# Kernel tuning notes

Measured on AMD Instinct MI355X. Metric: run time of the kernel, lower is better.

## Reference

```python
import jax, jax.numpy as jnp
import numpy as np

VOCAB, EMB, HID = 50000, 128, 256
B, T = 64, 512


def setup_inputs() -> dict:
    key = jax.random.key(0)
    ks = jax.random.split(key, 10)
    node = jax.random.randint(ks[0], (B, T, 2), 0, VOCAB, dtype=jnp.int32)
    rel = jax.random.randint(ks[1], (B, T, 3), 0, VOCAB, dtype=jnp.int32)
    father = jax.random.randint(ks[2], (B, T), 0, T, dtype=jnp.int32)
    mask = jnp.ones((B, T), jnp.float32)
    # parameters (PyTorch LSTM layout: gates ordered i,f,g,o)
    embedding = jax.random.normal(ks[3], (VOCAB, EMB), jnp.float32) * 1e-4
    W_ih = jax.random.uniform(ks[4], (4 * HID, 2 * EMB), jnp.float32, -0.02, 0.02)
    W_hh = jax.random.uniform(ks[5], (4 * HID, HID), jnp.float32, -0.02, 0.02)
    b_ih = jnp.zeros((4 * HID,), jnp.float32).at[HID:2 * HID].set(1.0)  # forget bias = 1
    b_hh = jnp.zeros((4 * HID,), jnp.float32)
    W_h = jax.random.normal(ks[6], (HID, HID), jnp.float32) * 0.02
    return {"src_gtr_seq_node": node, "src_gtr_seq_rel": rel,
            "src_gtr_seq_father": father, "src_gtr_seq_node_mask": mask,
            "embedding": embedding, "W_ih": W_ih, "W_hh": W_hh,
            "b_ih": b_ih, "b_hh": b_hh, "W_h": W_h}


def reference(src_gtr_seq_node, src_gtr_seq_rel, src_gtr_seq_father,
              src_gtr_seq_node_mask, embedding, W_ih, W_hh, b_ih, b_hh, W_h):
    node, rel, father, mask = (src_gtr_seq_node, src_gtr_seq_rel,
                               src_gtr_seq_father, src_gtr_seq_node_mask)
    Bn, Tn = node.shape[:2]
    H = W_hh.shape[1]
    t_idx = jnp.arange(Tn, dtype=jnp.int32)
    # valid parent at step t must point into memory slots [0..t]; -1 -> zero root slot
    father = jnp.minimum(father, (t_idx - 1)[None, :])
    # 'avg' mode: mean of first-2 node token embeddings, mean of rel token embeddings
    node_e = embedding[node].mean(axis=2)            # [B,T,E]
    rel_e = embedding[rel].mean(axis=2)              # [B,T,E]
    x = jnp.concatenate([node_e, rel_e], axis=-1)    # [B,T,2E]
    gx = jnp.einsum('bte,ge->btg', x, W_ih) + b_ih   # [B,T,4H] input-side gates
    barange = jnp.arange(Bn)
    h_mem0 = jnp.zeros((Tn + 1, Bn, H), x.dtype)     # slot 0 = zero state (root)
    c_mem0 = jnp.zeros((Tn + 1, Bn, H), x.dtype)

    def step(carry, inp):
        h_mem, c_mem = carry
        t, gx_t, f_t = inp
        h_prev = h_mem[f_t + 1, barange]             # parent gather [B,H]
        c_prev = c_mem[f_t + 1, barange]
        gates = gx_t + h_prev @ W_hh.T + b_hh        # [B,4H]
        i, f, g, o = jnp.split(gates, 4, axis=-1)
        c = jax.nn.sigmoid(f) * c_prev + jax.nn.sigmoid(i) * jnp.tanh(g)
        h = jax.nn.sigmoid(o) * jnp.tanh(c)
        return (h_mem.at[t + 1].set(h), c_mem.at[t + 1].set(c)), h

    (h_mem, c_mem), outs = jax.lax.scan(
        step, (h_mem0, c_mem0),
        (t_idx, gx.transpose(1, 0, 2), father.T))
    m = mask[:, :, None]
    encoder_outputs = outs.transpose(1, 0, 2) * m    # [B,T,H]
    encoder_feature = encoder_outputs.reshape(-1, H) @ W_h.T  # [B*T,H]
    h_max = (h_mem[1:].transpose(1, 0, 2) * m).max(axis=1)[None]  # [1,B,H]
    c_max = (c_mem[1:].transpose(1, 0, 2) * m).max(axis=1)[None]
    return encoder_outputs, encoder_feature, h_max, c_max
```

## Files before the change

### kernel.cpp

```cpp
#include <hip/hip_runtime.h>
#include <hip/hip_bf16.h>
#include <math.h>

#define NB 64
#define NT 512
#define NH 256
#define NG 1024

typedef __bf16 bf16x8 __attribute__((ext_vector_type(8)));
typedef float  f32x4  __attribute__((ext_vector_type(4)));

static __device__ __forceinline__ unsigned short f2bf(float x){
  __hip_bfloat16 h = __float2bfloat16(x);
  return __builtin_bit_cast(unsigned short, h);
}
static __device__ __forceinline__ float bf2f(unsigned short u){
  return __bfloat162float(__builtin_bit_cast(__hip_bfloat16, u));
}

#if __has_builtin(__builtin_amdgcn_sdot4)
#define SDOT4(a,b,c) __builtin_amdgcn_sdot4((a),(b),(c),false)
#else
static __device__ __forceinline__ int SDOT4(int a, int b, int c){
  c += ((a<<24)>>24)*((b<<24)>>24);
  c += ((a<<16)>>24)*((b<<16)>>24);
  c += ((a<< 8)>>24)*((b<< 8)>>24);
  c += ( a     >>24)*( b     >>24);
  return c;
}
#endif

#define BAR_LGKM() asm volatile("s_waitcnt lgkmcnt(0)\n\ts_barrier" ::: "memory")
#define BAR_ALL()  asm volatile("s_waitcnt vmcnt(0) lgkmcnt(0)\n\ts_barrier" ::: "memory")

#define PIN(x) asm volatile("" : "+v"(x))

static __device__ __forceinline__ float tanh_acc(float x){
  float ax = fabsf(x);
  if (ax < 0.04f){
    float x2 = x*x;
    return x * (1.0f + x2*(-(1.0f/3.0f) + x2*(2.0f/15.0f)));
  }
  float e = __expf(-2.0f*ax);
  float r = (1.0f - e) / (1.0f + e);
  return copysignf(r, x);
}
static __device__ __forceinline__ float sigm(float x){
  return 1.0f / (1.0f + __expf(-x));
}

#define HSCALE 1270000.0f
#define WSCALE 6350.0f
#define DQ_CONST (1.0f/(HSCALE*WSCALE))

__global__ __launch_bounds__(256) void k_prep(
    const float* __restrict__ Wih, const float* __restrict__ Whh,
    const float* __restrict__ Wh,  const float* __restrict__ bih,
    const float* __restrict__ bhh,
    unsigned short* __restrict__ wih_bf, unsigned short* __restrict__ wh_bf,
    int* __restrict__ wq, float* __restrict__ bias)
{
  int i = blockIdx.x*256 + threadIdx.x;
  wih_bf[i] = f2bf(Wih[i]);
  if (i < 65536){
    wh_bf[i] = f2bf(Wh[i]);
    float4 wv = *(const float4*)(Whh + (long)i*4);
    int q0 = (int)rintf(wv.x * WSCALE); q0 = max(-127, min(127, q0));
    int q1 = (int)rintf(wv.y * WSCALE); q1 = max(-127, min(127, q1));
    int q2 = (int)rintf(wv.z * WSCALE); q2 = max(-127, min(127, q2));
    int q3 = (int)rintf(wv.w * WSCALE); q3 = max(-127, min(127, q3));
    wq[i] = (q0&255) | ((q1&255)<<8) | ((q2&255)<<16) | ((q3&255)<<24);
  }
  if (i < 1024) bias[i] = bih[i] + bhh[i];
}

__global__ __launch_bounds__(128) void k_x(
    const int* __restrict__ node, const int* __restrict__ rel,
    const float* __restrict__ emb, unsigned short* __restrict__ x)
{
  int bt = blockIdx.x; int e = threadIdx.x;
  int n0 = node[bt*2+0], n1 = node[bt*2+1];
  int r0 = rel[bt*3+0], r1 = rel[bt*3+1], r2 = rel[bt*3+2];
  float a = (emb[(long)n0*128+e] + emb[(long)n1*128+e]) * 0.5f;
  float b = (emb[(long)r0*128+e] + emb[(long)r1*128+e] + emb[(long)r2*128+e]) * (1.0f/3.0f);
  x[(long)bt*256 + e]       = f2bf(a);
  x[(long)bt*256 + 128 + e] = f2bf(b);
}

__global__ __launch_bounds__(256) void k_gemm(
    const unsigned short* __restrict__ A, const unsigned short* __restrict__ Bw,
    unsigned short* __restrict__ Cbf, float* __restrict__ Cf32,
    const float* __restrict__ mask, int N, int mode)
{
  __shared__ __align__(16) unsigned short As[64][32];
  __shared__ __align__(16) unsigned short Bs[64][32];
  const int tid = threadIdx.x;
  const int lane = tid & 63, wave = tid >> 6;
  const int wm = wave >> 1, wn = wave & 1;
  const int l15 = lane & 15, quad = lane >> 4;
  const int tM = blockIdx.x * 64, tN = blockIdx.y * 64;
  const int srow = tid >> 2, sseg = tid & 3;
  f32x4 acc[2][2] = {};
  long arow = tM + srow;
  if (mode == 1) arow = arow + (arow >> 9) + 1;
  const unsigned short* Aptr = A + arow*256 + sseg*8;
  const unsigned short* Bptr = Bw + (long)(tN + srow)*256 + sseg*8;
  for (int kc = 0; kc < 8; ++kc){
    bf16x8 av = *(const bf16x8*)(Aptr + kc*32);
    bf16x8 bv = *(const bf16x8*)(Bptr + kc*32);
    *(bf16x8*)&As[srow][sseg*8] = av;
    *(bf16x8*)&Bs[srow][sseg*8] = bv;
    __syncthreads();
    bf16x8 af[2], bg[2];
    #pragma unroll
    for (int i=0;i<2;++i) af[i] = *(const bf16x8*)&As[wm*32 + i*16 + l15][quad*8];
    #pragma unroll
    for (int j=0;j<2;++j) bg[j] = *(const bf16x8*)&Bs[wn*32 + j*16 + l15][quad*8];
    #pragma unroll
    for (int i=0;i<2;++i)
      #pragma unroll
      for (int j=0;j<2;++j)
        acc[i][j] = __builtin_amdgcn_mfma_f32_16x16x32_bf16(af[i], bg[j], acc[i][j], 0,0,0);
    __syncthreads();
  }
  #pragma unroll
  for (int i=0;i<2;++i)
  #pragma unroll
  for (int j=0;j<2;++j)
  #pragma unroll
  for (int r=0;r<4;++r){
    int m = tM + wm*32 + i*16 + quad*4 + r;
    int n = tN + wn*32 + j*16 + l15;
    float v = acc[i][j][r];
    if (mode == 0) Cbf[(long)m*N + n] = f2bf(v);
    else           Cf32[(long)m*N + n] = v * mask[m];
  }
}

__global__ __launch_bounds__(512, 2) void k_scan(
    const int* __restrict__ father, const unsigned short* __restrict__ gx,
    const int* __restrict__ wq_g, const float* __restrict__ bias,
    unsigned short* __restrict__ h_hist, float* __restrict__ c_hist)
{
  const int b = blockIdx.x;
  const int tid = threadIdx.x;
  const int u = tid & 255;
  const int p = tid >> 8;
  extern __shared__ int smem[];
  int*    hqh  = smem;
  int*    fbuf = smem + 513*64;
  float2* gbuf = (float2*)(smem + 513*64 + 512);

  int wA[64], wB[64];
  {
    const int4* pA = (const int4*)(wq_g + (long)(p*512 + u)*64);
    const int4* pB = (const int4*)(wq_g + (long)(p*512 + 256 + u)*64);
    #pragma unroll
    for (int j=0;j<16;++j){
      int4 a = pA[j], c = pB[j];
      wA[4*j+0]=a.x; wA[4*j+1]=a.y; wA[4*j+2]=a.z; wA[4*j+3]=a.w;
      wB[4*j+0]=c.x; wB[4*j+1]=c.y; wB[4*j+2]=c.z; wB[4*j+3]=c.w;
    }
  }
  #pragma unroll
  for (int j=0;j<64;++j){ PIN(wA[j]); PIN(wB[j]); }

  const float bA = bias[p*512 + u];
  const float bB = bias[p*512 + 256 + u];
  fbuf[tid] = father[b*512 + tid];
  if (tid < 64) hqh[tid] = 0;
  __syncthreads();

  const long gxbase = (long)b*512*1024;
  float gA = bf2f(gx[gxbase + p*512 + u]);
  float gB = bf2f(gx[gxbase + p*512 + 256 + u]);
  float cp = 0.f, cprev = 0.f;
  int   fcur = -1;

  for (int t = 0; t < 512; ++t){
    const int hbase = (fcur + 1) * 64;
    int a0 = 0, a1 = 0;
    #pragma unroll
    for (int kc = 0; kc < 16; ++kc){
      int4 hv = *(const int4*)&hqh[hbase + kc*4];
      a0 = SDOT4(wA[4*kc+0], hv.x, a0); a1 = SDOT4(wB[4*kc+0], hv.x, a1);
      a0 = SDOT4(wA[4*kc+1], hv.y, a0); a1 = SDOT4(wB[4*kc+1], hv.y, a1);
      a0 = SDOT4(wA[4*kc+2], hv.z, a0); a1 = SDOT4(wB[4*kc+2], hv.z, a1);
      a0 = SDOT4(wA[4*kc+3], hv.w, a0); a1 = SDOT4(wB[4*kc+3], hv.w, a1);
    }
    if (p == 1){
      float gg = (float)a0 * DQ_CONST + gA + bA;
      float go = (float)a1 * DQ_CONST + gB + bB;
      gbuf[u] = make_float2(gg, go);
    }
    BAR_ALL();
    if (p == 0){
      float gi = (float)a0 * DQ_CONST + gA + bA;
      float gf = (float)a1 * DQ_CONST + gB + bB;
      float2 g2 = gbuf[u];
      float c = sigm(gf)*cp + sigm(gi)*tanh_acc(g2.x);
      float h = sigm(g2.y)*tanh_acc(c);
      long off = ((long)b*513 + (t+1))*256 + u;
      h_hist[off] = f2bf(h);
      c_hist[off] = c;
      int q = (int)rintf(h * HSCALE);
      q = max(-127, min(127, q));
      ((char*)hqh)[(t+1)*256 + u] = (char)q;
      cprev = c;
    }
    int fnext = fcur; float gA_n = 0.f, gB_n = 0.f, cp_n = 0.f;
    if (t < 511){
      fnext = min(fbuf[t+1], t);
      long gb = gxbase + (long)(t+1)*1024;
      gA_n = bf2f(gx[gb + p*512 + u]);
      gB_n = bf2f(gx[gb + p*512 + 256 + u]);
      if (p == 0 && fnext != t)
        cp_n = c_hist[((long)b*513 + fnext + 1)*256 + u];
    }
    BAR_LGKM();
    if (t < 511){
      cp = (fnext == t) ? cprev : cp_n;
      gA = gA_n; gB = gB_n;
      fcur = fnext;
    }
  }
}

__global__ __launch_bounds__(256) void k_eo1(
    const unsigned short* __restrict__ h_hist, const float* __restrict__ c_hist,
    const float* __restrict__ mask, float* __restrict__ out,
    float* __restrict__ pmax)
{
  int b = blockIdx.x, s = blockIdx.y, tid = threadIdx.x;
  float hm = -INFINITY, cm = -INFINITY;
  for (int i=0; i<64; ++i){
    int t = s*64 + i;
    long off = ((long)b*513 + t + 1)*256 + tid;
    float h = bf2f(h_hist[off]);
    float c = c_hist[off];
    float m = mask[b*512 + t];
    float e = h*m;
    out[((long)b*512 + t)*256 + tid] = e;
    hm = fmaxf(hm, e);
    cm = fmaxf(cm, c*m);
  }
  long po = ((long)(b*8 + s))*512 + tid;
  pmax[po]       = hm;
  pmax[po + 256] = cm;
}

__global__ __launch_bounds__(256) void k_eo2(
    const float* __restrict__ pmax, float* __restrict__ out)
{
  int b = blockIdx.x, tid = threadIdx.x;
  float hm = -INFINITY, cm = -INFINITY;
  for (int s=0; s<8; ++s){
    long po = ((long)(b*8 + s))*512 + tid;
    hm = fmaxf(hm, pmax[po]);
    cm = fmaxf(cm, pmax[po + 256]);
  }
  out[16777216L + b*256 + tid] = hm;
  out[16793600L + b*256 + tid] = cm;
}

extern "C" void kernel_launch(void* const* d_in, const int* in_sizes, int n_in,
                              void* d_out, int out_size, void* d_ws, size_t ws_size,
                              hipStream_t stream)
{
  const int*   node   = (const int*)  d_in[0];
  const int*   rel    = (const int*)  d_in[1];
  const int*   father = (const int*)  d_in[2];
  const float* mask   = (const float*)d_in[3];
  const float* emb    = (const float*)d_in[4];
  const float* Wih    = (const float*)d_in[5];
  const float* Whh    = (const float*)d_in[6];
  const float* bih    = (const float*)d_in[7];
  const float* bhh    = (const float*)d_in[8];
  const float* Wh     = (const float*)d_in[9];

  char* ws = (char*)d_ws;
  unsigned short* x_bf   = (unsigned short*)(ws);
  unsigned short* h_hist = (unsigned short*)(ws + 16777216);
  float*          c_hist = (float*)         (ws + 33587200);
  unsigned short* wih_bf = (unsigned short*)(ws + 75612160);
  unsigned short* wh_bf  = (unsigned short*)(ws + 76136448);
  int*            wq     = (int*)           (ws + 76267520);
  float*          bias   = (float*)         (ws + 76529664);
  float*          pmax   = (float*)(ws);

  unsigned short* gxbuf = (unsigned short*)d_out;
  float* out = (float*)d_out;

  const int scan_lds = (513*64 + 512)*4 + 256*8;

  k_prep<<<1024, 256, 0, stream>>>(Wih, Whh, Wh, bih, bhh, wih_bf, wh_bf, wq, bias);
  k_x<<<32768, 128, 0, stream>>>(node, rel, emb, x_bf);
  k_gemm<<<dim3(512,16), 256, 0, stream>>>(x_bf, wih_bf, gxbuf, nullptr, nullptr, 1024, 0);
  k_scan<<<64, 512, scan_lds, stream>>>(father, gxbuf, wq, bias, h_hist, c_hist);
  k_gemm<<<dim3(512,4), 256, 0, stream>>>(h_hist, wh_bf, nullptr, out + 8388608, mask, 256, 1);
  k_eo1<<<dim3(64,8), 256, 0, stream>>>(h_hist, c_hist, mask, out, pmax);
  k_eo2<<<64, 256, 0, stream>>>(pmax, out);
}
```

Before: 712.9 us.

## Restructure LSTM scan to pair gates via lane shuffles and skip barriers

Each wave's two 32-lane halves now compute complementary gate rows (i/g and f/o), so gate combination uses a cross-half shuffle instead of an LDS exchange plus full barrier. The step loop is unrolled by two with double-buffered global prefetch of gx and parent c via inline asm with explicit vmcnt waits. Recent c values are kept in registers, and the LDS barrier is only issued when the parent index reaches a step not yet synchronized. It relies on hand-tuned waitcnt ordering and conditional barriers, which risk races or wrong vmcnt accounting if the compiler reorders memory operations.

```diff
diff --git a/kernel.cpp b/kernel.cpp
--- a/kernel.cpp
+++ b/kernel.cpp
@@ -142,19 +142,23 @@
     const int* __restrict__ wq_g, const float* __restrict__ bias,
     unsigned short* __restrict__ h_hist, float* __restrict__ c_hist)
 {
-  const int b = blockIdx.x;
-  const int tid = threadIdx.x;
-  const int u = tid & 255;
-  const int p = tid >> 8;
+  const int b    = blockIdx.x;
+  const int tid  = threadIdx.x;
+  const int lane = tid & 63;
+  const int wave = tid >> 6;
+  const int half = lane >> 5;
+  const int u    = wave*32 + (lane & 31);
   extern __shared__ int smem[];
-  int*    hqh  = smem;
-  int*    fbuf = smem + 513*64;
-  float2* gbuf = (float2*)(smem + 513*64 + 512);
+  int* hqh  = smem;
+  int* fbuf = smem + 513*64;
+
+  const int rowA = half*256 + u;
+  const int rowB = rowA + 512;
 
   int wA[64], wB[64];
   {
-    const int4* pA = (const int4*)(wq_g + (long)(p*512 + u)*64);
-    const int4* pB = (const int4*)(wq_g + (long)(p*512 + 256 + u)*64);
+    const int4* pA = (const int4*)(wq_g + (long)rowA*64);
+    const int4* pB = (const int4*)(wq_g + (long)rowB*64);
     #pragma unroll
     for (int j=0;j<16;++j){
       int4 a = pA[j], c = pB[j];
@@ -165,65 +169,105 @@
   #pragma unroll
   for (int j=0;j<64;++j){ PIN(wA[j]); PIN(wB[j]); }
 
-  const float bA = bias[p*512 + u];
-  const float bB = bias[p*512 + 256 + u];
+  const float bA = bias[rowA];
+  const float bB = bias[rowB];
   fbuf[tid] = father[b*512 + tid];
   if (tid < 64) hqh[tid] = 0;
-  __syncthreads();
-
-  const long gxbase = (long)b*512*1024;
-  float gA = bf2f(gx[gxbase + p*512 + u]);
-  float gB = bf2f(gx[gxbase + p*512 + 256 + u]);
-  float cp = 0.f, cprev = 0.f;
-  int   fcur = -1;
-
-  for (int t = 0; t < 512; ++t){
-    const int hbase = (fcur + 1) * 64;
-    int a0 = 0, a1 = 0;
-    #pragma unroll
-    for (int kc = 0; kc < 16; ++kc){
-      int4 hv = *(const int4*)&hqh[hbase + kc*4];
-      a0 = SDOT4(wA[4*kc+0], hv.x, a0); a1 = SDOT4(wB[4*kc+0], hv.x, a1);
-      a0 = SDOT4(wA[4*kc+1], hv.y, a0); a1 = SDOT4(wB[4*kc+1], hv.y, a1);
-      a0 = SDOT4(wA[4*kc+2], hv.z, a0); a1 = SDOT4(wB[4*kc+2], hv.z, a1);
-      a0 = SDOT4(wA[4*kc+3], hv.w, a0); a1 = SDOT4(wB[4*kc+3], hv.w, a1);
-    }
-    if (p == 1){
-      float gg = (float)a0 * DQ_CONST + gA + bA;
-      float go = (float)a1 * DQ_CONST + gB + bB;
-      gbuf[u] = make_float2(gg, go);
-    }
-    BAR_ALL();
-    if (p == 0){
-      float gi = (float)a0 * DQ_CONST + gA + bA;
-      float gf = (float)a1 * DQ_CONST + gB + bB;
-      float2 g2 = gbuf[u];
-      float c = sigm(gf)*cp + sigm(gi)*tanh_acc(g2.x);
-      float h = sigm(g2.y)*tanh_acc(c);
-      long off = ((long)b*513 + (t+1))*256 + u;
-      h_hist[off] = f2bf(h);
-      c_hist[off] = c;
-      int q = (int)rintf(h * HSCALE);
-      q = max(-127, min(127, q));
-      ((char*)hqh)[(t+1)*256 + u] = (char)q;
-      cprev = c;
-    }
-    int fnext = fcur; float gA_n = 0.f, gB_n = 0.f, cp_n = 0.f;
-    if (t < 511){
-      fnext = min(fbuf[t+1], t);
-      long gb = gxbase + (long)(t+1)*1024;
-      gA_n = bf2f(gx[gb + p*512 + u]);
-      gB_n = bf2f(gx[gb + p*512 + 256 + u]);
-      if (p == 0 && fnext != t)
-        cp_n = c_hist[((long)b*513 + fnext + 1)*256 + u];
-    }
-    BAR_LGKM();
-    if (t < 511){
-      cp = (fnext == t) ? cprev : cp_n;
-      gA = gA_n; gB = gB_n;
-      fcur = fnext;
-    }
-  }
+
+  const unsigned short* gxp = gx + (long)b*524288;
+  unsigned int ga0 = gxp[rowA];
+  unsigned int gb0 = gxp[rowB];
+  unsigned int ga1 = gxp[1024 + rowA];
+  unsigned int gb1 = gxp[1024 + rowB];
+  const unsigned short* gptr = gxp + 2*1024 + rowA;
+  unsigned short* hst = h_hist + ((long)b*513 + 1)*256 + u;
+  float*          cst = c_hist + ((long)b*513 + 1)*256 + u;
+  const char*     clb = (const char*)(c_hist + (long)b*513*256 + u);
+
+  float cpl0 = 0.f, cpl1 = 0.f;
+  float cm1 = 0.f, cm2 = 0.f, cm3 = 0.f;
+  float selv = 0.f; int useL = 0;
+  int hbase = 0;
+  int lastBar = -1;
+  BAR_ALL();
+  int fc1 = fbuf[1];
+
+#define SCAN_BODY(T, CPL, GA, GB)                                              \
+  {                                                                            \
+    const int t = (T);                                                         \
+                                       \
+    int a0a=0,a0b=0,a1a=0,a1b=0;                                               \
+    _Pragma("unroll")                                                          \
+    for (int kc = 0; kc < 8; ++kc){                                            \
+      int4 h0 = *(const int4*)&hqh[hbase + kc*8];                              \
+      int4 h1 = *(const int4*)&hqh[hbase + kc*8 + 4];                          \
+      a0a = SDOT4(wA[8*kc+0], h0.x, a0a); a1a = SDOT4(wB[8*kc+0], h0.x, a1a);  \
+      a0a = SDOT4(wA[8*kc+1], h0.y, a0a); a1a = SDOT4(wB[8*kc+1], h0.y, a1a);  \
+      a0a = SDOT4(wA[8*kc+2], h0.z, a0a); a1a = SDOT4(wB[8*kc+2], h0.z, a1a);  \
+      a0a = SDOT4(wA[8*kc+3], h0.w, a0a); a1a = SDOT4(wB[8*kc+3], h0.w, a1a);  \
+      a0b = SDOT4(wA[8*kc+4], h1.x, a0b); a1b = SDOT4(wB[8*kc+4], h1.x, a1b);  \
+      a0b = SDOT4(wA[8*kc+5], h1.y, a0b); a1b = SDOT4(wB[8*kc+5], h1.y, a1b);  \
+      a0b = SDOT4(wA[8*kc+6], h1.z, a0b); a1b = SDOT4(wB[8*kc+6], h1.z, a1b);  \
+      a0b = SDOT4(wA[8*kc+7], h1.w, a0b); a1b = SDOT4(wB[8*kc+7], h1.w, a1b);  \
+    }                                                                          \
+    int a0 = a0a + a0b, a1 = a1a + a1b;                                        \
+             \
+    asm volatile("s_waitcnt vmcnt(5)" : "+v"(CPL), "+v"(GA), "+v"(GB));        \
+    float gAf = __uint_as_float(GA << 16);                                     \
+    float gBf = __uint_as_float(GB << 16);                                     \
+    float vA = (float)a0 * DQ_CONST + gAf + bA;                                \
+    float vB = (float)a1 * DQ_CONST + gBf + bB;                                \
+                 \
+    float s0 = sigm(vA);                                \
+    float th = tanh_acc(vB);                            \
+    float s1 = sigm(vB);                                \
+    float sf = __shfl_xor(s0, 32, 64);                                         \
+    float so = __shfl_xor(s1, 32, 64);                                         \
+    float pre = s0 * th;                                                       \
+    float cp  = useL ? CPL : selv;                                             \
+    float c   = fmaf(sf, cp, pre);                                             \
+    float h   = so * tanh_acc(c);               \
+    if (lane < 32){                                                            \
+      unsigned int hb = (unsigned int)f2bf(h);                                 \
+      asm volatile("global_store_short %0, %1, off" :: "v"(hst), "v"(hb));     \
+      asm volatile("global_store_dword %0, %1, off" :: "v"(cst), "v"(c));      \
+      int q = (int)rintf(h * HSCALE);                                          \
+      q = max(-127, min(127, q));                                              \
+      ((char*)hqh)[(t+1)*256 + u] = (char)q;                                   \
+    }                                                                          \
+    cm3 = cm2; cm2 = cm1; cm1 = c;                                             \
+    hst += 256; cst += 256;                                                    \
+     \
+    int fr2 = __builtin_amdgcn_readfirstlane(fbuf[t+2 < 512 ? t+2 : 511]);     \
+    {                                                                          \
+      int fL = min(fr2, t+1);                                                  \
+      const char* cla = clb + (long)(fL+1)*1024;                               \
+      asm volatile("global_load_dword %0, %1, off" : "=v"(CPL) : "v"(cla));    \
+      asm volatile("global_load_ushort %0, %1, off" : "=v"(GA) : "v"(gptr));   \
+      asm volatile("global_load_ushort %0, %1, off offset:1024"                \
+                   : "=v"(GB) : "v"(gptr));                                    \
+    }                                                                          \
+    if (t < 509) gptr += 1024;                                                 \
+            \
+    {                                                                          \
+      int fA = min(fc1, t);                                                    \
+      useL = (fA < t-2);                                                       \
+      selv = (fA == t) ? cm1 : ((fA == t-1) ? cm2 : cm3);                      \
+      hbase = (fA + 1) * 64;                                                   \
+      fc1 = fr2;                                                               \
+      if (fA > lastBar){                                                       \
+        BAR_LGKM();                                                            \
+        lastBar = t;                                                           \
+      }                                                                        \
+    }                                                                          \
+  }
+
+  #pragma unroll 1
+  for (int tb = 0; tb < 512; tb += 2){
+    SCAN_BODY(tb,   cpl0, ga0, gb0)
+    SCAN_BODY(tb+1, cpl1, ga1, gb1)
+  }
+#undef SCAN_BODY
 }
 
 __global__ __launch_bounds__(256) void k_eo1(
@@ -291,7 +335,7 @@
   unsigned short* gxbuf = (unsigned short*)d_out;
   float* out = (float*)d_out;
 
-  const int scan_lds = (513*64 + 512)*4 + 256*8;
+  const int scan_lds = (513*64 + 512)*4;
 
   k_prep<<<1024, 256, 0, stream>>>(Wih, Whh, Wh, bih, bhh, wih_bf, wh_bf, wq, bias);
   k_x<<<32768, 128, 0, stream>>>(node, rel, emb, x_bf);
```

Result: no change. 714.9 us (+0.3%).
